# Kernel tuning notes

Measured on AMD Instinct MI355X. Metric: run time of the kernel, lower is better.

## Reference

```python
import jax, jax.numpy as jnp
import numpy as np
import math

B, L, NH, HD = 2, 2048, 8, 128
C = NH * HD            # hidden size
K = 3                  # short_conv_L
EMB, ORDER = 33, 64    # hyena filter emb_dim / order


def setup_inputs() -> dict:
    key = jax.random.key(0)
    ks = jax.random.split(key, 10)
    f32 = jnp.float32
    return {
        "query_layer": jax.random.normal(ks[0], (L, B, NH, HD), f32),
        "key_layer": jax.random.normal(ks[1], (L, B, NH, HD), f32),
        "value_layer": jax.random.normal(ks[2], (L, B, NH, HD), f32),
        # depthwise short conv params: [3(qkv), C, 1, K] / [3, C]
        "short_conv_weight": jax.random.normal(ks[3], (3, C, 1, K), f32) * 0.3,
        "short_conv_bias": jax.random.normal(ks[4], (3, C), f32) * 0.02,
        # D term of the long conv, shape [head_dim]
        "long_conv_bias": jax.random.normal(ks[5], (HD,), f32) * 0.1,
        # hyena filter MLP (torch Linear convention: W [out, in])
        "lin0_w": jax.random.normal(ks[6], (ORDER, EMB), f32) * (1.0 / np.sqrt(EMB)),
        "lin0_b": jnp.zeros((ORDER,), f32),
        "lin1_w": jax.random.normal(ks[7], (ORDER, ORDER), f32) * (1.0 / np.sqrt(ORDER)),
        "lin1_b": jnp.zeros((ORDER,), f32),
        "lin2_w": jax.random.normal(ks[8], (ORDER, ORDER), f32) * (1.0 / np.sqrt(ORDER)),
        "lin2_b": jnp.zeros((ORDER,), f32),
        "freq": jnp.ones((1, ORDER), f32),  # Sin activation freq (w=1), shared across layers
        "final_w": jax.random.normal(ks[9], (HD, ORDER), f32) * (1.0 / np.sqrt(ORDER)),
        # exponential modulation decay rates, [1,1,HD], as initialized in the module
        "mod_weight": jnp.linspace(math.log(0.01) / 1.5, math.log(0.01) / 0.3, HD,
                                   dtype=f32)[None, None],
    }


def _depthwise_conv(x, w, b):
    # x [B,C,L], w [C,1,K], b [C]; causal: pad K-1 both sides, keep first L
    y = jax.lax.conv_general_dilated(
        x, w, window_strides=(1,), padding=[(K - 1, K - 1)],
        feature_group_count=C, dimension_numbers=("NCH", "OIH", "NCH"))
    return y[..., :L] + b[None, :, None]


def _hyena_filter(lin0_w, lin0_b, lin1_w, lin1_b, lin2_w, lin2_b, freq, final_w, mod_weight):
    t = jnp.linspace(0.0, 1.0, L)[None, :, None]              # [1,L,1]
    bands = (EMB - 1) // 2
    w_ang = 2.0 * jnp.pi * jnp.linspace(0.0, L - 1.0, L) / L  # [L]
    f = jnp.linspace(1e-4, bands - 1.0, bands)                # [bands]
    theta = w_ang[:, None] * f[None, :]                       # [L,bands]; z = exp(-1j f w)
    z = jnp.concatenate([t[0], jnp.cos(theta), -jnp.sin(theta)], axis=-1)[None]  # [1,L,EMB]
    h = jnp.sin(freq * (z @ lin0_w.T + lin0_b))
    h = jnp.sin(freq * (h @ lin1_w.T + lin1_b))
    h = jnp.sin(freq * (h @ lin2_w.T + lin2_b))
    h = h @ final_w.T                                         # [1,L,HD]
    h = h * jnp.exp(-t * jnp.abs(mod_weight))                 # exponential modulation
    return h[0].T                                             # [HD, L]


def _fftconv_heads(k, kern, D, q, v):
    # mirrors fftconv_heads_ref with head_dim=NH: channels split as (h=HD, d=NH)
    b = k.shape[0]
    kr = k.reshape(b, HD, NH, L).transpose(0, 2, 1, 3)  # b nh hd L  (d1 axis)
    vr = v.reshape(b, HD, NH, L).transpose(0, 2, 1, 3)  # b nh hd L  (d2 axis)
    qr = q.reshape(b, HD, NH, L).transpose(0, 2, 1, 3)  # b nh hd L
    kv = kr[:, :, None] * vr[:, None]                   # [b, nh, nh, hd, L]
    n = 2 * L
    kv_f = jnp.fft.rfft(kv, n=n) / n
    kern_f = jnp.fft.rfft(kern, n=n)                    # [HD, n//2+1]
    y = jnp.fft.irfft(kv_f * kern_f, n=n, norm="forward")[..., :L]
    out = y + kv * D[:, None]                           # D over head_dim axis
    out = (out * qr[:, :, None]).sum(axis=1)            # _mul_sum over d1 -> [b, nh, hd, L]
    return out.transpose(0, 2, 1, 3).reshape(b, C, L)   # 'b d2 h l -> b (h d2) l'


def reference(query_layer, key_layer, value_layer, short_conv_weight, short_conv_bias,
              long_conv_bias, lin0_w, lin0_b, lin1_w, lin1_b, lin2_w, lin2_b,
              freq, final_w, mod_weight):
    # 'sq b np hn -> b (np hn) sq'
    q = jnp.transpose(query_layer, (1, 2, 3, 0)).reshape(B, C, L)
    k = jnp.transpose(key_layer, (1, 2, 3, 0)).reshape(B, C, L)
    v = jnp.transpose(value_layer, (1, 2, 3, 0)).reshape(B, C, L)
    q = _depthwise_conv(q, short_conv_weight[0], short_conv_bias[0])
    k = _depthwise_conv(k, short_conv_weight[1], short_conv_bias[1])
    v = _depthwise_conv(v, short_conv_weight[2], short_conv_bias[2])
    filt = _hyena_filter(lin0_w, lin0_b, lin1_w, lin1_b, lin2_w, lin2_b,
                         freq, final_w, mod_weight)
    # module calls fftconv_heads_ref(k=value, ..., q=query, v=key)
    y = _fftconv_heads(v, filt, long_conv_bias, q=q, v=k)
    # 'b (np hn) sq -> b np sq hn'
    return y.reshape(B, NH, HD, L).transpose(0, 1, 3, 2)
```

## Files before the change

kernel.cpp:

```cpp
#include <hip/hip_runtime.h>
#include <stdint.h>

#define L_SEQ 2048
#define B_SZ 2
#define NHH 8
#define HDD 128
#define C_SZ 1024
#define EMB_D 33
#define ORD 64
#define BANDS 16
#define FSTRIDE (L_SEQ + 256)
#define FRS_S 2600
#define FRS_FILL 2176
#define QTS 136

typedef _Float16 f16;
typedef f16 f16x8 __attribute__((ext_vector_type(8)));
typedef float f32x4 __attribute__((ext_vector_type(4)));

__global__ void filter_kernel(const float* __restrict__ w0, const float* __restrict__ b0,
                              const float* __restrict__ w1, const float* __restrict__ b1,
                              const float* __restrict__ w2, const float* __restrict__ b2,
                              const float* __restrict__ fr, const float* __restrict__ wf,
                              const float* __restrict__ md, const float* __restrict__ Dv,
                              float* __restrict__ filt) {
  int tid = threadIdx.x;
  int o = tid & 63;
  int lq = tid >> 6;
  int l = blockIdx.x * 4 + lq;

  if (blockIdx.x < 128) filt[(size_t)blockIdx.x * FSTRIDE + tid] = 0.0f;

  __shared__ float zs[4][EMB_D];
  __shared__ float hs[4][ORD];
  __shared__ float gs[4][ORD];

  float t = (float)l / (float)(L_SEQ - 1);
  float wang = 6.2831853071795864f * (float)l / (float)L_SEQ;
  const float fstep = (15.0f - 1e-4f) / 15.0f;

  if (o == 0) zs[lq][0] = t;
  if (o >= 1 && o < 1 + BANDS) {
    int j = o - 1;
    float fj = 1e-4f + fstep * (float)j;
    zs[lq][1 + j] = cosf(wang * fj);
  }
  if (o >= 1 + BANDS && o < 1 + 2 * BANDS) {
    int j = o - 1 - BANDS;
    float fj = 1e-4f + fstep * (float)j;
    zs[lq][1 + BANDS + j] = -sinf(wang * fj);
  }
  __syncthreads();

  float fo = fr[o];
  float a = b0[o];
  for (int e = 0; e < EMB_D; ++e) a += zs[lq][e] * w0[o * EMB_D + e];
  hs[lq][o] = sinf(fo * a);
  __syncthreads();

  a = b1[o];
  for (int e = 0; e < ORD; ++e) a += hs[lq][e] * w1[o * ORD + e];
  gs[lq][o] = sinf(fo * a);
  __syncthreads();

  a = b2[o];
  for (int e = 0; e < ORD; ++e) a += gs[lq][e] * w2[o * ORD + e];
  float h3 = sinf(fo * a);
  __syncthreads();
  hs[lq][o] = h3;
  __syncthreads();

  #pragma unroll
  for (int pass = 0; pass < 2; ++pass) {
    int hd = pass * 64 + o;
    float acc = 0.0f;
    for (int e = 0; e < ORD; ++e) acc += hs[lq][e] * wf[hd * ORD + e];
    float val = acc * expf(-t * fabsf(md[hd]));
    if (l == 0) val += Dv[hd];
    filt[(size_t)hd * FSTRIDE + 256 + l] = val;
  }
}

#define TLC 64
__global__ void shortconv_kernel(const float* __restrict__ q_in,
                                 const float* __restrict__ k_in,
                                 const float* __restrict__ v_in,
                                 const float* __restrict__ scw,
                                 const float* __restrict__ scb,
                                 float* __restrict__ Aq, f16* __restrict__ Akt16,
                                 f16* __restrict__ Avt16) {
  int bid = blockIdx.x;
  int lt = bid & 31;
  int np = (bid >> 5) & 7;
  int b = bid >> 8;
  int l0 = lt * TLC;
  int tid = threadIdx.x;

  __shared__ float xs[TLC + 2][HDD + 4];
  __shared__ float wcs[HDD][4];

  const float* ins[3] = {q_in, k_in, v_in};

  for (int tsr = 0; tsr < 3; ++tsr) {
    const float* x = ins[tsr];
    if (tid < HDD) {
      int c = np * HDD + tid;
      wcs[tid][0] = scw[(tsr * C_SZ + c) * 3 + 0];
      wcs[tid][1] = scw[(tsr * C_SZ + c) * 3 + 1];
      wcs[tid][2] = scw[(tsr * C_SZ + c) * 3 + 2];
      wcs[tid][3] = scb[tsr * C_SZ + c];
    }
    for (int idx = tid; idx < (TLC + 2) * HDD; idx += 256) {
      int row = idx >> 7, hn = idx & 127;
      int l = l0 - 2 + row;
      float val = 0.0f;
      if (l >= 0) val = x[(((size_t)l * B_SZ + b) * NHH + np) * HDD + hn];
      xs[row][hn] = val;
    }
    __syncthreads();

    int n1 = tid & 7;
    int lp = tid >> 3;
    for (int hdi = 0; hdi < 16; ++hdi) {
      int hn = hdi * 8 + n1;
      float cw0 = wcs[hn][0], cw1 = wcs[hn][1], cw2 = wcs[hn][2], cb = wcs[hn][3];
      int hd = np * 16 + hdi;
      #pragma unroll
      for (int half = 0; half < 2; ++half) {
        int ll = half * 32 + lp;
        float y = cb + cw0 * xs[ll][hn] + cw1 * xs[ll + 1][hn]
                     + cw2 * xs[ll + 2][hn];
        int l = l0 + ll;
        if (tsr == 0) {
          Aq[(((size_t)b * HDD + hd) * L_SEQ + l) * NHH + n1] = y;
        } else {
          int ch = l >> 7, m = l & 127;
          int off = (n1 << 8) | ((m << 1) ^ (n1 << 4));
          char* base = (tsr == 1) ? (char*)Akt16 : (char*)Avt16;
          *(f16*)(base + ((((size_t)(b * HDD + hd)) * 16 + ch) << 11) + off) = (f16)y;
        }
      }
    }
    __syncthreads();
  }
}

__global__ void __launch_bounds__(256, 2)
hyena_main(const float* __restrict__ Aq, const f16* __restrict__ Akt16,
           const f16* __restrict__ Avt16, const float* __restrict__ filt,
           float* __restrict__ out) {
  int bid = blockIdx.x;
  int g  = bid & 1;
  int hd = (bid >> 1) & 127;
  int b  = bid >> 8;
  int tid = threadIdx.x;
  int w = tid >> 6;
  int lane = tid & 63;
  int r = lane & 15;
  int p = lane >> 4;
  int a = (15 - r) & 7;

  __shared__ f16 FRS[8][FRS_S];
  __shared__ f16 AV[2][1024];
  __shared__ f16 AK[2][1024];
  __shared__ float Qt[4][8][QTS];

  const float* frow = filt + (size_t)hd * FSTRIDE + 256;
  const float* aqb = Aq + ((size_t)b * HDD + hd) * (size_t)L_SEQ * NHH;
  const char* avtg = (const char*)Avt16 + (((size_t)(b * HDD + hd)) * 16 << 11);
  const char* aktg = (const char*)Akt16 + (((size_t)(b * HDD + hd)) * 16 << 11);
  int np = hd >> 4, hnb = (hd & 15) * 8;

  for (int aa = 0; aa < 8; ++aa)
    for (int z = tid; z < FRS_FILL; z += 256)
      FRS[aa][z] = (f16)frow[2047 - z - aa];

  f32x4 acc[8][4];

  auto dma = [&](int c, int bi) {
    const char* srcb = (w >> 1) ? aktg : avtg;
    f16* dstb = (w >> 1) ? &AK[bi][(w & 1) * 512] : &AV[bi][(w & 1) * 512];
    const char* src = srcb + ((size_t)c << 11) + (w & 1) * 1024 + lane * 16;
    __builtin_amdgcn_global_load_lds((const unsigned int*)src,
                                     (unsigned int*)dstb, 16, 0, 0);
  };

  auto stage_qt = [&](int l0) {
    const float4* src = (const float4*)(aqb + (size_t)l0 * 8);
    #pragma unroll
    for (int rr = 0; rr < 2; ++rr) {
      int i = rr * 64 + lane;
      float4 q0 = src[i * 2], q1 = src[i * 2 + 1];
      Qt[w][0][i] = q0.x; Qt[w][1][i] = q0.y; Qt[w][2][i] = q0.z; Qt[w][3][i] = q0.w;
      Qt[w][4][i] = q1.x; Qt[w][5][i] = q1.y; Qt[w][6][i] = q1.z; Qt[w][7][i] = q1.w;
    }
  };

  auto unit = [&](int lt, int c, int bi) {
    int dy = 2047 - (lt - c) * 128;
    int zbase = dy - r - a + p * 8 - 112;
    f16x8 f[14];
    #pragma unroll
    for (int dd = 0; dd < 14; ++dd)
      f[dd] = *(const f16x8*)&FRS[a][zbase + 16 * dd];
    int ky = r & 7;
    #pragma unroll
    for (int s = 0; s < 4; ++s) {
      f16x8 kf = *(const f16x8*)&AK[bi][ky * 128 + ((s * 32 + p * 8) ^ (ky * 8))];
      #pragma unroll
      for (int nt = 0; nt < 4; ++nt) {
        int vy = nt * 2 + (r >> 3);
        f16x8 vf = *(const f16x8*)&AV[bi][vy * 128 + ((s * 32 + p * 8) ^ (vy * 8))];
        f16x8 bf = vf * kf;
        #pragma unroll
        for (int mt = 0; mt < 8; ++mt)
          acc[mt][nt] = __builtin_amdgcn_mfma_f32_16x16x32_f16(
              f[7 + 2 * s - mt], bf, acc[mt][nt], 0, 0, 0);
      }
    }
  };

  auto epilogue = [&](int lt) {
    int l0 = lt * 128;
    int hi = r >> 3;
    int n2 = r & 7;
    #pragma unroll
    for (int mt = 0; mt < 8; ++mt) {
      float4 qv[4];
      #pragma unroll
      for (int nt = 0; nt < 4; ++nt)
        qv[nt] = *(const float4*)&Qt[w][nt * 2 + hi][mt * 16 + p * 4];
      #pragma unroll
      for (int reg = 0; reg < 4; ++reg) {
        float pr = qv[0][reg] * acc[mt][0][reg] + qv[1][reg] * acc[mt][1][reg]
                 + qv[2][reg] * acc[mt][2][reg] + qv[3][reg] * acc[mt][3][reg];
        pr += __shfl_xor(pr, 8, 64);
        if (r < 8) {
          int i = mt * 16 + p * 4 + reg;
          out[(((size_t)b * NHH + np) * L_SEQ + (l0 + i)) * HDD + hnb + n2] = pr;
        }
      }
    }
  };

  auto run_pass = [&](int mytile, int NC) {
    dma(0, 0);
    stage_qt(mytile * 128);
    #pragma unroll
    for (int mt = 0; mt < 8; ++mt)
      #pragma unroll
      for (int nt = 0; nt < 4; ++nt)
        acc[mt][nt] = f32x4{0.f, 0.f, 0.f, 0.f};
    for (int c = 0; c < NC; ++c) {
      __syncthreads();
      if (c + 1 < NC) dma(c + 1, (c + 1) & 1);
      if (mytile >= c) unit(mytile, c, c & 1);
      if (mytile == c) epilogue(mytile);
    }
    __syncthreads();
  };

  run_pass(g * 4 + w, g * 4 + 4);
  run_pass(15 - g * 4 - w, 16 - g * 4);
}

extern "C" void kernel_launch(void* const* d_in, const int* in_sizes, int n_in,
                              void* d_out, int out_size, void* d_ws, size_t ws_size,
                              hipStream_t stream) {
  const float* q_in = (const float*)d_in[0];
  const float* k_in = (const float*)d_in[1];
  const float* v_in = (const float*)d_in[2];
  const float* scw  = (const float*)d_in[3];
  const float* scb  = (const float*)d_in[4];
  const float* Dv   = (const float*)d_in[5];
  const float* w0   = (const float*)d_in[6];
  const float* b0   = (const float*)d_in[7];
  const float* w1   = (const float*)d_in[8];
  const float* b1   = (const float*)d_in[9];
  const float* w2   = (const float*)d_in[10];
  const float* b2   = (const float*)d_in[11];
  const float* fr   = (const float*)d_in[12];
  const float* wf   = (const float*)d_in[13];
  const float* md   = (const float*)d_in[14];

  float* ws   = (float*)d_ws;
  float* filt = ws;
  float* Aq   = ws + (size_t)HDD * FSTRIDE;
  f16*   Akt16 = (f16*)(Aq + (size_t)B_SZ * HDD * L_SEQ * NHH);
  f16*   Avt16 = Akt16 + (size_t)B_SZ * HDD * 16 * 1024;

  filter_kernel<<<512, 256, 0, stream>>>(w0, b0, w1, b1, w2, b2, fr, wf, md, Dv, filt);
  shortconv_kernel<<<512, 256, 0, stream>>>(q_in, k_in, v_in, scw, scb, Aq, Akt16, Avt16);
  hyena_main<<<512, 256, 0, stream>>>(Aq, Akt16, Avt16, filt, (float*)d_out);
}
```

Baseline: 156.6 us.

## Split output tiles across waves and blocks, read Q transposed directly from global

The main kernel now launches 2048 blocks instead of 512. Each block handles one tile pair, and the four waves split each output tile's eight m-subtiles between them, so every wave holds 2x4 accumulators instead of 8x4. This cuts register pressure, which allows 3 blocks per CU, and adds parallelism. The short-conv kernel writes Q in a transposed layout so the epilogue can load it directly from global memory, removing the LDS Qt staging. The trade-off is that every block must rebuild the full 8-copy filter table in shared memory, four times as many times in total, and the K and V chunks are re-streamed per block; the MFMA loop is also raised to a higher scheduling priority.

```diff
diff --git a/kernel.cpp b/kernel.cpp
--- a/kernel.cpp
+++ b/kernel.cpp
@@ -12,7 +12,6 @@
 #define FSTRIDE (L_SEQ + 256)
 #define FRS_S 2600
 #define FRS_FILL 2176
-#define QTS 136
 
 typedef _Float16 f16;
 typedef f16 f16x8 __attribute__((ext_vector_type(8)));
@@ -87,7 +86,7 @@
                                  const float* __restrict__ v_in,
                                  const float* __restrict__ scw,
                                  const float* __restrict__ scb,
-                                 float* __restrict__ Aq, f16* __restrict__ Akt16,
+                                 float* __restrict__ AqT, f16* __restrict__ Akt16,
                                  f16* __restrict__ Avt16) {
   int bid = blockIdx.x;
   int lt = bid & 31;
@@ -132,7 +131,7 @@
                      + cw2 * xs[ll + 2][hn];
         int l = l0 + ll;
         if (tsr == 0) {
-          Aq[(((size_t)b * HDD + hd) * L_SEQ + l) * NHH + n1] = y;
+          AqT[(((size_t)b * HDD + hd) * NHH + n1) * L_SEQ + l] = y;
         } else {
           int ch = l >> 7, m = l & 127;
           int off = (n1 << 8) | ((m << 1) ^ (n1 << 4));
@@ -145,14 +144,14 @@
   }
 }
 
-__global__ void __launch_bounds__(256, 2)
-hyena_main(const float* __restrict__ Aq, const f16* __restrict__ Akt16,
+__global__ void __launch_bounds__(256, 3)
+hyena_main(const float* __restrict__ AqT, const f16* __restrict__ Akt16,
            const f16* __restrict__ Avt16, const float* __restrict__ filt,
            float* __restrict__ out) {
   int bid = blockIdx.x;
-  int g  = bid & 1;
-  int hd = (bid >> 1) & 127;
-  int b  = bid >> 8;
+  int pr = bid & 7;
+  int hd = (bid >> 3) & 127;
+  int b  = bid >> 10;
   int tid = threadIdx.x;
   int w = tid >> 6;
   int lane = tid & 63;
@@ -163,19 +162,18 @@
   __shared__ f16 FRS[8][FRS_S];
   __shared__ f16 AV[2][1024];
   __shared__ f16 AK[2][1024];
-  __shared__ float Qt[4][8][QTS];
 
   const float* frow = filt + (size_t)hd * FSTRIDE + 256;
-  const float* aqb = Aq + ((size_t)b * HDD + hd) * (size_t)L_SEQ * NHH;
   const char* avtg = (const char*)Avt16 + (((size_t)(b * HDD + hd)) * 16 << 11);
   const char* aktg = (const char*)Akt16 + (((size_t)(b * HDD + hd)) * 16 << 11);
+  const float* aqtb = AqT + ((size_t)b * HDD + hd) * NHH * L_SEQ;
   int np = hd >> 4, hnb = (hd & 15) * 8;
 
   for (int aa = 0; aa < 8; ++aa)
     for (int z = tid; z < FRS_FILL; z += 256)
       FRS[aa][z] = (f16)frow[2047 - z - aa];
 
-  f32x4 acc[8][4];
+  f32x4 acc[2][4];
 
   auto dma = [&](int c, int bi) {
     const char* srcb = (w >> 1) ? aktg : avtg;
@@ -185,25 +183,15 @@
                                      (unsigned int*)dstb, 16, 0, 0);
   };
 
-  auto stage_qt = [&](int l0) {
-    const float4* src = (const float4*)(aqb + (size_t)l0 * 8);
-    #pragma unroll
-    for (int rr = 0; rr < 2; ++rr) {
-      int i = rr * 64 + lane;
-      float4 q0 = src[i * 2], q1 = src[i * 2 + 1];
-      Qt[w][0][i] = q0.x; Qt[w][1][i] = q0.y; Qt[w][2][i] = q0.z; Qt[w][3][i] = q0.w;
-      Qt[w][4][i] = q1.x; Qt[w][5][i] = q1.y; Qt[w][6][i] = q1.z; Qt[w][7][i] = q1.w;
-    }
-  };
-
   auto unit = [&](int lt, int c, int bi) {
     int dy = 2047 - (lt - c) * 128;
-    int zbase = dy - r - a + p * 8 - 112;
-    f16x8 f[14];
-    #pragma unroll
-    for (int dd = 0; dd < 14; ++dd)
-      f[dd] = *(const f16x8*)&FRS[a][zbase + 16 * dd];
+    int zb = dy - r - a + p * 8 - 112 + 16 * (3 - w);
+    f16x8 f[6];
+    #pragma unroll
+    for (int j = 0; j < 6; ++j)
+      f[j] = *(const f16x8*)&FRS[a][zb + 32 * j];
     int ky = r & 7;
+    __builtin_amdgcn_s_setprio(1);
     #pragma unroll
     for (int s = 0; s < 4; ++s) {
       f16x8 kf = *(const f16x8*)&AK[bi][ky * 128 + ((s * 32 + p * 8) ^ (ky * 8))];
@@ -212,12 +200,13 @@
         int vy = nt * 2 + (r >> 3);
         f16x8 vf = *(const f16x8*)&AV[bi][vy * 128 + ((s * 32 + p * 8) ^ (vy * 8))];
         f16x8 bf = vf * kf;
-        #pragma unroll
-        for (int mt = 0; mt < 8; ++mt)
-          acc[mt][nt] = __builtin_amdgcn_mfma_f32_16x16x32_f16(
-              f[7 + 2 * s - mt], bf, acc[mt][nt], 0, 0, 0);
+        acc[0][nt] = __builtin_amdgcn_mfma_f32_16x16x32_f16(
+            f[s + 2], bf, acc[0][nt], 0, 0, 0);
+        acc[1][nt] = __builtin_amdgcn_mfma_f32_16x16x32_f16(
+            f[s], bf, acc[1][nt], 0, 0, 0);
       }
     }
+    __builtin_amdgcn_s_setprio(0);
   };
 
   auto epilogue = [&](int lt) {
@@ -225,43 +214,44 @@
     int hi = r >> 3;
     int n2 = r & 7;
     #pragma unroll
-    for (int mt = 0; mt < 8; ++mt) {
+    for (int mi = 0; mi < 2; ++mi) {
+      int mt = w + 4 * mi;
       float4 qv[4];
       #pragma unroll
       for (int nt = 0; nt < 4; ++nt)
-        qv[nt] = *(const float4*)&Qt[w][nt * 2 + hi][mt * 16 + p * 4];
+        qv[nt] = *(const float4*)(aqtb + (size_t)(nt * 2 + hi) * L_SEQ
+                                  + l0 + mt * 16 + p * 4);
       #pragma unroll
       for (int reg = 0; reg < 4; ++reg) {
-        float pr = qv[0][reg] * acc[mt][0][reg] + qv[1][reg] * acc[mt][1][reg]
-                 + qv[2][reg] * acc[mt][2][reg] + qv[3][reg] * acc[mt][3][reg];
-        pr += __shfl_xor(pr, 8, 64);
+        float pv = qv[0][reg] * acc[mi][0][reg] + qv[1][reg] * acc[mi][1][reg]
+                 + qv[2][reg] * acc[mi][2][reg] + qv[3][reg] * acc[mi][3][reg];
+        pv += __shfl_xor(pv, 8, 64);
         if (r < 8) {
           int i = mt * 16 + p * 4 + reg;
-          out[(((size_t)b * NHH + np) * L_SEQ + (l0 + i)) * HDD + hnb + n2] = pr;
+          out[(((size_t)b * NHH + np) * L_SEQ + (l0 + i)) * HDD + hnb + n2] = pv;
         }
       }
     }
   };
 
-  auto run_pass = [&](int mytile, int NC) {
+  auto run_pass = [&](int lt, int NC) {
+    #pragma unroll
+    for (int mi = 0; mi < 2; ++mi)
+      #pragma unroll
+      for (int nt = 0; nt < 4; ++nt)
+        acc[mi][nt] = f32x4{0.f, 0.f, 0.f, 0.f};
     dma(0, 0);
-    stage_qt(mytile * 128);
-    #pragma unroll
-    for (int mt = 0; mt < 8; ++mt)
-      #pragma unroll
-      for (int nt = 0; nt < 4; ++nt)
-        acc[mt][nt] = f32x4{0.f, 0.f, 0.f, 0.f};
     for (int c = 0; c < NC; ++c) {
       __syncthreads();
       if (c + 1 < NC) dma(c + 1, (c + 1) & 1);
-      if (mytile >= c) unit(mytile, c, c & 1);
-      if (mytile == c) epilogue(mytile);
-    }
+      unit(lt, c, c & 1);
+    }
+    epilogue(lt);
     __syncthreads();
   };
 
-  run_pass(g * 4 + w, g * 4 + 4);
-  run_pass(15 - g * 4 - w, 16 - g * 4);
+  run_pass(pr, pr + 1);
+  run_pass(15 - pr, 16 - pr);
 }
 
 extern "C" void kernel_launch(void* const* d_in, const int* in_sizes, int n_in,
@@ -285,11 +275,11 @@
 
   float* ws   = (float*)d_ws;
   float* filt = ws;
-  float* Aq   = ws + (size_t)HDD * FSTRIDE;
-  f16*   Akt16 = (f16*)(Aq + (size_t)B_SZ * HDD * L_SEQ * NHH);
+  float* AqT  = ws + (size_t)HDD * FSTRIDE;
+  f16*   Akt16 = (f16*)(AqT + (size_t)B_SZ * HDD * L_SEQ * NHH);
   f16*   Avt16 = Akt16 + (size_t)B_SZ * HDD * 16 * 1024;
 
   filter_kernel<<<512, 256, 0, stream>>>(w0, b0, w1, b1, w2, b2, fr, wf, md, Dv, filt);
-  shortconv_kernel<<<512, 256, 0, stream>>>(q_in, k_in, v_in, scw, scb, Aq, Akt16, Avt16);
-  hyena_main<<<512, 256, 0, stream>>>(Aq, Akt16, Avt16, filt, (float*)d_out);
-}
+  shortconv_kernel<<<512, 256, 0, stream>>>(q_in, k_in, v_in, scw, scb, AqT, Akt16, Avt16);
+  hyena_main<<<2048, 256, 0, stream>>>(AqT, Akt16, Avt16, filt, (float*)d_out);
+}
```

Result: slower. 163.2 us (+4.2%).

## Precompute shifted fp16 filter globally and decouple waves with per-wave async pipelines

Applied to the files above, without the earlier changes.

A new prep kernel builds the eight shifted fp16 filter copies in global memory once, so the main kernel no longer fills a large LDS filter table per block and reads filter fragments straight from global/L2. Each wave now has private double-buffered K/V LDS tiles loaded with global_load_lds and waits on vmcnt instead of block-wide __syncthreads, running both tile passes in one fused loop. Q is stored as transposed fp16 and read directly in the epilogue, and the block index mapping is reordered so blocks sharing a head run close together. In exchange it adds an extra launch, more global filter traffic, lower Q precision, and duplicated K/V loads across the four waves.

```diff
diff --git a/kernel.cpp b/kernel.cpp
--- a/kernel.cpp
+++ b/kernel.cpp
@@ -1,5 +1,6 @@
 #include <hip/hip_runtime.h>
 #include <stdint.h>
+#include <string.h>
 
 #define L_SEQ 2048
 #define B_SZ 2
@@ -10,12 +11,11 @@
 #define ORD 64
 #define BANDS 16
 #define FSTRIDE (L_SEQ + 256)
-#define FRS_S 2600
-#define FRS_FILL 2176
-#define QTS 136
+#define FRSG_S 2176
 
 typedef _Float16 f16;
 typedef f16 f16x8 __attribute__((ext_vector_type(8)));
+typedef f16 f16x4 __attribute__((ext_vector_type(4)));
 typedef float f32x4 __attribute__((ext_vector_type(4)));
 
 __global__ void filter_kernel(const float* __restrict__ w0, const float* __restrict__ b0,
@@ -81,13 +81,22 @@
   }
 }
 
+__global__ void frs_prep(const float* __restrict__ filt, f16* __restrict__ FRSg) {
+  int hd = blockIdx.x;
+  int tid = threadIdx.x;
+  const float* frow = filt + (size_t)hd * FSTRIDE + 256;
+  for (int a = 0; a < 8; ++a)
+    for (int z = tid; z < FRSG_S; z += 256)
+      FRSg[((size_t)hd * 8 + a) * FRSG_S + z] = (f16)frow[2047 - z - a];
+}
+
 #define TLC 64
 __global__ void shortconv_kernel(const float* __restrict__ q_in,
                                  const float* __restrict__ k_in,
                                  const float* __restrict__ v_in,
                                  const float* __restrict__ scw,
                                  const float* __restrict__ scb,
-                                 float* __restrict__ Aq, f16* __restrict__ Akt16,
+                                 f16* __restrict__ AqT16, f16* __restrict__ Akt16,
                                  f16* __restrict__ Avt16) {
   int bid = blockIdx.x;
   int lt = bid & 31;
@@ -132,7 +141,7 @@
                      + cw2 * xs[ll + 2][hn];
         int l = l0 + ll;
         if (tsr == 0) {
-          Aq[(((size_t)b * HDD + hd) * L_SEQ + l) * NHH + n1] = y;
+          AqT16[(((size_t)b * HDD + hd) * NHH + n1) * L_SEQ + l] = (f16)y;
         } else {
           int ch = l >> 7, m = l & 127;
           int off = (n1 << 8) | ((m << 1) ^ (n1 << 4));
@@ -146,13 +155,13 @@
 }
 
 __global__ void __launch_bounds__(256, 2)
-hyena_main(const float* __restrict__ Aq, const f16* __restrict__ Akt16,
-           const f16* __restrict__ Avt16, const float* __restrict__ filt,
+hyena_main(const f16* __restrict__ AqT16, const f16* __restrict__ Akt16,
+           const f16* __restrict__ Avt16, const f16* __restrict__ FRSg,
            float* __restrict__ out) {
   int bid = blockIdx.x;
-  int g  = bid & 1;
-  int hd = (bid >> 1) & 127;
-  int b  = bid >> 8;
+  int g  = bid >> 8;
+  int hd = bid & 127;
+  int b  = (bid >> 7) & 1;
   int tid = threadIdx.x;
   int w = tid >> 6;
   int lane = tid & 63;
@@ -160,57 +169,105 @@
   int p = lane >> 4;
   int a = (15 - r) & 7;
 
-  __shared__ f16 FRS[8][FRS_S];
-  __shared__ f16 AV[2][1024];
-  __shared__ f16 AK[2][1024];
-  __shared__ float Qt[4][8][QTS];
-
-  const float* frow = filt + (size_t)hd * FSTRIDE + 256;
-  const float* aqb = Aq + ((size_t)b * HDD + hd) * (size_t)L_SEQ * NHH;
+  __shared__ f16 AVp[4][2][1024];
+  __shared__ f16 AKp[4][2][1024];
+
   const char* avtg = (const char*)Avt16 + (((size_t)(b * HDD + hd)) * 16 << 11);
   const char* aktg = (const char*)Akt16 + (((size_t)(b * HDD + hd)) * 16 << 11);
+  const f16* aqtb = AqT16 + ((size_t)b * HDD + hd) * NHH * L_SEQ;
+  const f16* aflane = FRSg + (size_t)hd * 8 * FRSG_S + a * FRSG_S
+                      - (r + a) + 8 * p - 112;
   int np = hd >> 4, hnb = (hd & 15) * 8;
 
-  for (int aa = 0; aa < 8; ++aa)
-    for (int z = tid; z < FRS_FILL; z += 256)
-      FRS[aa][z] = (f16)frow[2047 - z - aa];
-
   f32x4 acc[8][4];
+  #pragma unroll
+  for (int mt = 0; mt < 8; ++mt)
+    #pragma unroll
+    for (int nt = 0; nt < 4; ++nt) acc[mt][nt] = f32x4{0.f, 0.f, 0.f, 0.f};
 
   auto dma = [&](int c, int bi) {
-    const char* srcb = (w >> 1) ? aktg : avtg;
-    f16* dstb = (w >> 1) ? &AK[bi][(w & 1) * 512] : &AV[bi][(w & 1) * 512];
-    const char* src = srcb + ((size_t)c << 11) + (w & 1) * 1024 + lane * 16;
-    __builtin_amdgcn_global_load_lds((const unsigned int*)src,
-                                     (unsigned int*)dstb, 16, 0, 0);
+    #pragma unroll
+    for (int seg = 0; seg < 2; ++seg) {
+      __builtin_amdgcn_global_load_lds(
+          (const unsigned int*)(avtg + ((size_t)c << 11) + seg * 1024 + lane * 16),
+          (unsigned int*)&AVp[w][bi][seg * 512], 16, 0, 0);
+      __builtin_amdgcn_global_load_lds(
+          (const unsigned int*)(aktg + ((size_t)c << 11) + seg * 1024 + lane * 16),
+          (unsigned int*)&AKp[w][bi][seg * 512], 16, 0, 0);
+    }
   };
 
-  auto stage_qt = [&](int l0) {
-    const float4* src = (const float4*)(aqb + (size_t)l0 * 8);
-    #pragma unroll
-    for (int rr = 0; rr < 2; ++rr) {
-      int i = rr * 64 + lane;
-      float4 q0 = src[i * 2], q1 = src[i * 2 + 1];
-      Qt[w][0][i] = q0.x; Qt[w][1][i] = q0.y; Qt[w][2][i] = q0.z; Qt[w][3][i] = q0.w;
-      Qt[w][4][i] = q1.x; Qt[w][5][i] = q1.y; Qt[w][6][i] = q1.z; Qt[w][7][i] = q1.w;
+  auto epilogue = [&](int lt) {
+    int l0 = lt * 128;
+    int hi = r >> 3;
+    int n2 = r & 7;
+    #pragma unroll
+    for (int mt = 0; mt < 8; ++mt) {
+      f16x4 qh[4];
+      #pragma unroll
+      for (int nt = 0; nt < 4; ++nt)
+        qh[nt] = *(const f16x4*)(aqtb + (size_t)(nt * 2 + hi) * L_SEQ
+                                 + l0 + mt * 16 + p * 4);
+      #pragma unroll
+      for (int reg = 0; reg < 4; ++reg) {
+        float pv = (float)qh[0][reg] * acc[mt][0][reg]
+                 + (float)qh[1][reg] * acc[mt][1][reg]
+                 + (float)qh[2][reg] * acc[mt][2][reg]
+                 + (float)qh[3][reg] * acc[mt][3][reg];
+        pv += __shfl_xor(pv, 8, 64);
+        if (r < 8) {
+          int i = mt * 16 + p * 4 + reg;
+          out[(((size_t)b * NHH + np) * L_SEQ + (l0 + i)) * HDD + hnb + n2] = pv;
+        }
+      }
     }
   };
 
-  auto unit = [&](int lt, int c, int bi) {
+  int tA = g * 4 + w;
+  int tB = 15 - tA;
+  int NCa = tA + 1;
+
+  dma(0, 0);
+  f16x8 f[14];
+
+  for (int i = 0; i < 17; ++i) {
+    int ti = (i >= NCa);
+    int lt = ti ? tB : tA;
+    int c  = ti ? i - NCa : i;
+
+    if (i == NCa) {
+      epilogue(tA);
+      #pragma unroll
+      for (int mt = 0; mt < 8; ++mt)
+        #pragma unroll
+        for (int nt = 0; nt < 4; ++nt) acc[mt][nt] = f32x4{0.f, 0.f, 0.f, 0.f};
+    }
+
     int dy = 2047 - (lt - c) * 128;
-    int zbase = dy - r - a + p * 8 - 112;
-    f16x8 f[14];
-    #pragma unroll
-    for (int dd = 0; dd < 14; ++dd)
-      f[dd] = *(const f16x8*)&FRS[a][zbase + 16 * dd];
+    const f16* fb = aflane + dy;
+    #pragma unroll
+    for (int dd = 0; dd < 14; ++dd) f[dd] = *(const f16x8*)(fb + 16 * dd);
+
+    if (i + 1 < 17) {
+      int i2 = i + 1;
+      int c2 = (i2 >= NCa) ? i2 - NCa : i2;
+      dma(c2, i2 & 1);
+      asm volatile("s_waitcnt vmcnt(4)" ::: "memory");
+    } else {
+      asm volatile("s_waitcnt vmcnt(0)" ::: "memory");
+    }
+    __builtin_amdgcn_sched_barrier(0);
+
+    int bi = i & 1;
     int ky = r & 7;
+    __builtin_amdgcn_s_setprio(1);
     #pragma unroll
     for (int s = 0; s < 4; ++s) {
-      f16x8 kf = *(const f16x8*)&AK[bi][ky * 128 + ((s * 32 + p * 8) ^ (ky * 8))];
+      f16x8 kf = *(const f16x8*)&AKp[w][bi][ky * 128 + ((s * 32 + p * 8) ^ (ky * 8))];
       #pragma unroll
       for (int nt = 0; nt < 4; ++nt) {
         int vy = nt * 2 + (r >> 3);
-        f16x8 vf = *(const f16x8*)&AV[bi][vy * 128 + ((s * 32 + p * 8) ^ (vy * 8))];
+        f16x8 vf = *(const f16x8*)&AVp[w][bi][vy * 128 + ((s * 32 + p * 8) ^ (vy * 8))];
         f16x8 bf = vf * kf;
         #pragma unroll
         for (int mt = 0; mt < 8; ++mt)
@@ -218,50 +275,10 @@
               f[7 + 2 * s - mt], bf, acc[mt][nt], 0, 0, 0);
       }
     }
-  };
-
-  auto epilogue = [&](int lt) {
-    int l0 = lt * 128;
-    int hi = r >> 3;
-    int n2 = r & 7;
-    #pragma unroll
-    for (int mt = 0; mt < 8; ++mt) {
-      float4 qv[4];
-      #pragma unroll
-      for (int nt = 0; nt < 4; ++nt)
-        qv[nt] = *(const float4*)&Qt[w][nt * 2 + hi][mt * 16 + p * 4];
-      #pragma unroll
-      for (int reg = 0; reg < 4; ++reg) {
-        float pr = qv[0][reg] * acc[mt][0][reg] + qv[1][reg] * acc[mt][1][reg]
-                 + qv[2][reg] * acc[mt][2][reg] + qv[3][reg] * acc[mt][3][reg];
-        pr += __shfl_xor(pr, 8, 64);
-        if (r < 8) {
-          int i = mt * 16 + p * 4 + reg;
-          out[(((size_t)b * NHH + np) * L_SEQ + (l0 + i)) * HDD + hnb + n2] = pr;
-        }
-      }
-    }
-  };
-
-  auto run_pass = [&](int mytile, int NC) {
-    dma(0, 0);
-    stage_qt(mytile * 128);
-    #pragma unroll
-    for (int mt = 0; mt < 8; ++mt)
-      #pragma unroll
-      for (int nt = 0; nt < 4; ++nt)
-        acc[mt][nt] = f32x4{0.f, 0.f, 0.f, 0.f};
-    for (int c = 0; c < NC; ++c) {
-      __syncthreads();
-      if (c + 1 < NC) dma(c + 1, (c + 1) & 1);
-      if (mytile >= c) unit(mytile, c, c & 1);
-      if (mytile == c) epilogue(mytile);
-    }
-    __syncthreads();
-  };
-
-  run_pass(g * 4 + w, g * 4 + 4);
-  run_pass(15 - g * 4 - w, 16 - g * 4);
+    __builtin_amdgcn_s_setprio(0);
+  }
+
+  epilogue(tB);
 }
 
 extern "C" void kernel_launch(void* const* d_in, const int* in_sizes, int n_in,
@@ -283,13 +300,15 @@
   const float* wf   = (const float*)d_in[13];
   const float* md   = (const float*)d_in[14];
 
-  float* ws   = (float*)d_ws;
-  float* filt = ws;
-  float* Aq   = ws + (size_t)HDD * FSTRIDE;
-  f16*   Akt16 = (f16*)(Aq + (size_t)B_SZ * HDD * L_SEQ * NHH);
-  f16*   Avt16 = Akt16 + (size_t)B_SZ * HDD * 16 * 1024;
+  float* ws    = (float*)d_ws;
+  float* filt  = ws;
+  f16* AqT16   = (f16*)(ws + (size_t)HDD * FSTRIDE);
+  f16* Akt16   = AqT16 + (size_t)B_SZ * HDD * NHH * L_SEQ;
+  f16* Avt16   = Akt16 + (size_t)B_SZ * HDD * 16 * 1024;
+  f16* FRSg    = Avt16 + (size_t)B_SZ * HDD * 16 * 1024;
 
   filter_kernel<<<512, 256, 0, stream>>>(w0, b0, w1, b1, w2, b2, fr, wf, md, Dv, filt);
-  shortconv_kernel<<<512, 256, 0, stream>>>(q_in, k_in, v_in, scw, scb, Aq, Akt16, Avt16);
-  hyena_main<<<512, 256, 0, stream>>>(Aq, Akt16, Avt16, filt, (float*)d_out);
-}
+  frs_prep<<<128, 256, 0, stream>>>(filt, FRSg);
+  shortconv_kernel<<<512, 256, 0, stream>>>(q_in, k_in, v_in, scw, scb, AqT16, Akt16, Avt16);
+  hyena_main<<<512, 256, 0, stream>>>(AqT16, Akt16, Avt16, FRSg, (float*)d_out);
+}
```

Result: slower. 223.7 us (+42.8%).
